# Optimization experiments

Measured on AMD Instinct MI355X. Metric: run time of the kernel, lower is better.

Reference implementation:

```python
import jax, jax.numpy as jnp
import numpy as np


def _2div(arr):
    arr_res = arr.copy()
    arr_pieces = []
    pa = 0
    st = 0
    needdivcnt = 0
    for i, a in enumerate(arr):
        if a != pa:
            arr_pieces.append([st, i])
            if i - st != 1:
                needdivcnt += 1
            pa = a
            st = i
    arr_pieces.append([st, len(arr)])
    if len(arr) - st != 1:
        needdivcnt += 1
    offset = range(len(arr_pieces), len(arr_pieces) + needdivcnt)
    p = 0
    for arr_p in arr_pieces:
        length = arr_p[1] - arr_p[0]
        if length == 1:
            continue
        half_len = int(np.ceil(length / 2))
        for j in range(arr_p[0] + half_len, arr_p[1]):
            arr_res[j] = offset[p]
        p += 1
    return arr_res


def get_division_tree(n_agents):
    agent2divitreeindex = np.arange(n_agents)
    np.random.shuffle(agent2divitreeindex)
    max_div = np.ceil(np.log2(n_agents)).astype(int)
    levels = np.zeros(shape=(max_div + 1, n_agents), dtype=int)
    for ith in range(1, len(levels)):
        levels[ith, :] = _2div(levels[ith - 1, :])
    res_levels = levels.copy()
    for i, idx in enumerate(agent2divitreeindex):
        res_levels[:, i] = levels[:, idx]
    return res_levels


def setup_inputs() -> dict:
    B, A, H, NACT = 2048, 50, 512, 64
    F = H + A  # in-features of first Linear (hidden + one-hot agent id)
    np.random.seed(0)
    div_tree = get_division_tree(A)
    routing = jnp.asarray(div_tree[-1], dtype=jnp.int32)  # max_level routing: agent -> net index
    key = jax.random.key(0)
    k0, k1, k2 = jax.random.split(key, 3)
    x_in = jax.random.normal(k0, (B, A, H), dtype=jnp.float32)
    # stacked per-net parameters (n_nets == n_agent independent 2-layer MLPs)
    W1 = jax.random.normal(k1, (A, F, H), dtype=jnp.float32) * (1.0 / np.sqrt(F))
    b1 = jnp.zeros((A, H), dtype=jnp.float32)
    W2 = jax.random.normal(k2, (A, H, NACT), dtype=jnp.float32) * (1.0 / np.sqrt(H))
    b2 = jnp.zeros((A, NACT), dtype=jnp.float32)
    return {"x_in": x_in, "W1": W1, "b1": b1, "W2": W2, "b2": b2, "routing": routing}


def reference(x_in, W1, b1, W2, b2, routing):
    # x_in: [B, A, H]; routing: [A] int (which net each agent uses)
    B, A, H = x_in.shape
    # add_onehot_id_at_last_dim: append agent-id one-hot -> [B, A, H+A]
    onehot = jnp.broadcast_to(jnp.eye(A, dtype=x_in.dtype), (B, A, A))
    x0 = jnp.concatenate([x_in, onehot], axis=-1)
    # gather routed expert weights per agent
    W1r, b1r = W1[routing], b1[routing]   # [A, H+A, H], [A, H]
    W2r, b2r = W2[routing], b2[routing]   # [A, H, NACT], [A, NACT]
    h = jax.nn.relu(jnp.einsum('baf,afh->bah', x0, W1r) + b1r)
    out = jnp.einsum('bah,ahn->ban', h, W2r) + b2r  # [B, A, NACT]
    return out
```

## Files before the change

### kernel.cpp

```cpp
#include <hip/hip_runtime.h>

typedef __attribute__((ext_vector_type(8))) short bf16x8;
typedef __attribute__((ext_vector_type(4))) float f32x4;
typedef __attribute__((ext_vector_type(4))) unsigned short u16x4;
typedef __attribute__((ext_vector_type(8))) unsigned short u16x8;

#define B_ 2048
#define A_ 50
#define H_ 512
#define NACT_ 64
#define F_ 562
#define BM_ 128
#define BK_ 32
#define NSTEP_ (H_ / BK_)
#define W1LD_ (BK_ + 8)
#define HLD_ (H_ + 8)

#define WS_W1T 0
#define WS_W2T ((size_t)A_ * H_ * H_ * 2)
#define WS_B1 (WS_W2T + (size_t)A_ * NACT_ * H_ * 2)
#define WS_B2 (WS_B1 + (size_t)A_ * H_ * 4)

static __device__ __forceinline__ unsigned short f2bf(float f) {
  unsigned int u = __builtin_bit_cast(unsigned int, f);
  u += 0x7fffu + ((u >> 16) & 1u);
  return (unsigned short)(u >> 16);
}

static __device__ __forceinline__ void gld_lds16(const unsigned short* src,
                                                 unsigned short* dst) {
  __builtin_amdgcn_global_load_lds(
      (const __attribute__((address_space(1))) unsigned int*)(const void*)src,
      (__attribute__((address_space(3))) unsigned int*)(void*)dst, 16, 0, 0);
}

static __device__ __forceinline__ int clamp_r(int r) {
  return r < 0 ? 0 : (r > A_ - 1 ? A_ - 1 : r);
}

__global__ void prep_w1(const float* __restrict__ w1,
                        const int* __restrict__ routing,
                        unsigned short* __restrict__ w1t) {
  const int bid = blockIdx.x;
  const int a = bid / 64;
  const int tile = bid - a * 64;
  const int tk = tile & 7, tj = tile >> 3;
  const int k0 = tk * 64, j0 = tj * 64;
  const int r = clamp_r(routing[a]);
  __shared__ float tl[64][65];
  const int t = threadIdx.x;
  const int c = t & 63, q = t >> 6;
#pragma unroll
  for (int i = 0; i < 16; ++i) {
    const int kl = q + i * 4;
    tl[kl][c] = w1[((size_t)r * F_ + k0 + kl) * H_ + j0 + c];
  }
  __syncthreads();
#pragma unroll
  for (int i = 0; i < 16; ++i) {
    const int jl = q + i * 4;
    w1t[((size_t)a * H_ + j0 + jl) * H_ + k0 + c] = f2bf(tl[c][jl]);
  }
}

__global__ void prep_w2(const float* __restrict__ w2,
                        const int* __restrict__ routing,
                        unsigned short* __restrict__ w2t) {
  const int bid = blockIdx.x;
  const int a = bid >> 3;
  const int tk = bid & 7;
  const int k0 = tk * 64;
  const int r = clamp_r(routing[a]);
  __shared__ float tl[64][65];
  const int t = threadIdx.x;
  const int c = t & 63, q = t >> 6;
#pragma unroll
  for (int i = 0; i < 16; ++i) {
    const int kl = q + i * 4;
    tl[kl][c] = w2[((size_t)r * H_ + k0 + kl) * NACT_ + c];
  }
  __syncthreads();
#pragma unroll
  for (int i = 0; i < 16; ++i) {
    const int nl = q + i * 4;
    w2t[((size_t)a * NACT_ + nl) * H_ + k0 + c] = f2bf(tl[c][nl]);
  }
}

__global__ void prep_bias(const float* __restrict__ w1,
                          const float* __restrict__ b1,
                          const float* __restrict__ b2,
                          const int* __restrict__ routing,
                          float* __restrict__ bias1, float* __restrict__ bias2) {
  const int a = blockIdx.x;
  const int t = threadIdx.x;
  const int r = clamp_r(routing[a]);
  bias1[a * H_ + t] = b1[(size_t)r * H_ + t] + w1[((size_t)r * F_ + H_ + a) * H_ + t];
  if (t < NACT_) bias2[a * NACT_ + t] = b2[r * NACT_ + t];
}

__global__ __launch_bounds__(512, 2) void divtree_main(
    const float* __restrict__ x, const unsigned short* __restrict__ w1t,
    const unsigned short* __restrict__ w2t, const float* __restrict__ bias1,
    const float* __restrict__ bias2, float* __restrict__ out) {
  __shared__ union {
    struct {
      unsigned short w1[2][H_ * W1LD_];
      unsigned short xs[2][BM_ * W1LD_];
    } st;
    unsigned short h[BM_ * HLD_];
  } sm;

  const int bid = blockIdx.x;
  const int swz = (bid & 7) * 100 + (bid >> 3);
  const int a = swz >> 4;
  const int mblk = swz & 15;
  const int b0 = mblk * BM_;

  const int tid = threadIdx.x;
  const int lane = tid & 63;
  const int w = tid >> 6;
  const int l16 = lane & 15;
  const int lk = lane >> 4;

  const int wj = (w & 3) * 128;
  const int wm = (w >> 2) * 64;

  const unsigned short* w1ta = w1t + (size_t)a * H_ * H_;

  const int xrow = tid >> 2;
  const int xc = (tid & 3) * 8;
  const float* xbase =
      x + ((size_t)b0 * A_ + (size_t)a) * H_ + (size_t)xrow * (A_ * H_) + xc;

  f32x4 acc[8][4];
#pragma unroll
  for (int i = 0; i < 8; ++i)
#pragma unroll
    for (int j = 0; j < 4; ++j) acc[i][j] = (f32x4){0.f, 0.f, 0.f, 0.f};

  f32x4 xv0, xv1;

  {
    xv0 = *(const f32x4*)(xbase);
    xv1 = *(const f32x4*)(xbase + 4);
#pragma unroll
    for (int i = 0; i < 5; ++i) {
      const int chunk = i * 512 + tid;
      const int j = chunk / 5;
      const int part = chunk - j * 5;
      const unsigned short* src =
          (part < 4) ? (w1ta + (size_t)j * H_ + part * 8) : w1ta;
      unsigned short* dst = sm.st.w1[0] + (size_t)(i * 512 + (w << 6)) * 8;
      gld_lds16(src, dst);
    }
    u16x8 v;
#pragma unroll
    for (int e = 0; e < 4; ++e) v[e] = f2bf(xv0[e]);
#pragma unroll
    for (int e = 0; e < 4; ++e) v[4 + e] = f2bf(xv1[e]);
    *(u16x8*)(sm.st.xs[0] + xrow * W1LD_ + xc) = v;
  }
  __syncthreads();

  int cur = 0;
  for (int t = 0; t < NSTEP_; ++t) {
    const bool pf = (t + 1 < NSTEP_);
    if (pf) {
      const float* p = xbase + (t + 1) * BK_;
      xv0 = *(const f32x4*)p;
      xv1 = *(const f32x4*)(p + 4);
      const int k0 = (t + 1) * BK_;
#pragma unroll
      for (int i = 0; i < 5; ++i) {
        const int chunk = i * 512 + tid;
        const int j = chunk / 5;
        const int part = chunk - j * 5;
        const unsigned short* src =
            (part < 4) ? (w1ta + (size_t)j * H_ + k0 + part * 8) : w1ta;
        unsigned short* dst =
            sm.st.w1[cur ^ 1] + (size_t)(i * 512 + (w << 6)) * 8;
        gld_lds16(src, dst);
      }
    }
    const unsigned short* w1s = sm.st.w1[cur];
    const unsigned short* xss = sm.st.xs[cur];
    bf16x8 afr[8], bfr[4];
#pragma unroll
    for (int jf = 0; jf < 8; ++jf)
      afr[jf] = *(const bf16x8*)(w1s + (wj + jf * 16 + l16) * W1LD_ + lk * 8);
#pragma unroll
    for (int mf = 0; mf < 4; ++mf)
      bfr[mf] = *(const bf16x8*)(xss + (wm + mf * 16 + l16) * W1LD_ + lk * 8);
#pragma unroll
    for (int jf = 0; jf < 8; ++jf)
#pragma unroll
      for (int mf = 0; mf < 4; ++mf)
        acc[jf][mf] = __builtin_amdgcn_mfma_f32_16x16x32_bf16(
            afr[jf], bfr[mf], acc[jf][mf], 0, 0, 0);
    if (pf) {
      u16x8 v;
#pragma unroll
      for (int e = 0; e < 4; ++e) v[e] = f2bf(xv0[e]);
#pragma unroll
      for (int e = 0; e < 4; ++e) v[4 + e] = f2bf(xv1[e]);
      *(u16x8*)(sm.st.xs[cur ^ 1] + xrow * W1LD_ + xc) = v;
    }
    __syncthreads();
    cur ^= 1;
  }

  const float* b1p = bias1 + a * H_;
#pragma unroll
  for (int jf = 0; jf < 8; ++jf) {
    const f32x4 bv = *(const f32x4*)(b1p + wj + jf * 16 + lk * 4);
#pragma unroll
    for (int mf = 0; mf < 4; ++mf) {
      u16x4 hv;
#pragma unroll
      for (int r = 0; r < 4; ++r) {
        float f = acc[jf][mf][r] + bv[r];
        f = f > 0.f ? f : 0.f;
        hv[r] = f2bf(f);
      }
      const int m = wm + mf * 16 + l16;
      const int j0 = wj + jf * 16 + lk * 4;
      *(u16x4*)(sm.h + (size_t)m * HLD_ + j0) = hv;
    }
  }
  __syncthreads();

  const int n2 = (w & 3) * 16;
  const int m2 = (w >> 2) * 64;
  const unsigned short* w2p =
      w2t + ((size_t)a * NACT_ + n2 + l16) * H_ + lk * 8;
  f32x4 acc2[4];
#pragma unroll
  for (int mf = 0; mf < 4; ++mf) acc2[mf] = (f32x4){0.f, 0.f, 0.f, 0.f};
#pragma unroll
  for (int ks = 0; ks < 16; ++ks) {
    const bf16x8 bf2 = *(const bf16x8*)(w2p + ks * 32);
#pragma unroll
    for (int mf = 0; mf < 4; ++mf) {
      const bf16x8 af2 = *(const bf16x8*)(
          sm.h + (size_t)(m2 + mf * 16 + l16) * HLD_ + ks * 32 + lk * 8);
      acc2[mf] = __builtin_amdgcn_mfma_f32_16x16x32_bf16(af2, bf2, acc2[mf],
                                                         0, 0, 0);
    }
  }
  const float b2v = bias2[a * NACT_ + n2 + l16];
#pragma unroll
  for (int mf = 0; mf < 4; ++mf)
#pragma unroll
    for (int r = 0; r < 4; ++r) {
      const int m = m2 + mf * 16 + lk * 4 + r;
      out[((size_t)(b0 + m) * A_ + a) * NACT_ + n2 + l16] = acc2[mf][r] + b2v;
    }
}

extern "C" void kernel_launch(void* const* d_in, const int* in_sizes, int n_in,
                              void* d_out, int out_size, void* d_ws,
                              size_t ws_size, hipStream_t stream) {
  const float* x = (const float*)d_in[0];
  const float* w1 = (const float*)d_in[1];
  const float* b1 = (const float*)d_in[2];
  const float* w2 = (const float*)d_in[3];
  const float* b2 = (const float*)d_in[4];
  const int* routing = (const int*)d_in[5];
  float* out = (float*)d_out;

  char* ws = (char*)d_ws;
  unsigned short* w1t = (unsigned short*)(ws + WS_W1T);
  unsigned short* w2t = (unsigned short*)(ws + WS_W2T);
  float* bias1 = (float*)(ws + WS_B1);
  float* bias2 = (float*)(ws + WS_B2);

  prep_w1<<<A_ * 64, 256, 0, stream>>>(w1, routing, w1t);
  prep_w2<<<A_ * 8, 256, 0, stream>>>(w2, routing, w2t);
  prep_bias<<<A_, 512, 0, stream>>>(w1, b1, b2, routing, bias1, bias2);
  divtree_main<<<A_ * (B_ / BM_), 512, 0, stream>>>(x, w1t, w2t, bias1, bias2,
                                                    out);
}
```

Baseline: 157.9 us.

## Halve batch tile, pre-tile W1 with XOR swizzle, drop LDS padding for occupancy

The prep kernel now writes W1 in a K-tiled layout where each 32-wide K slice is contiguous and 8-element chunks are XOR-swizzled by row. The main kernel can then load each stage with plain linear global-to-LDS copies and read fragments without bank conflicts, and no padded LDS rows are needed. The batch tile drops from 128 to 64 rows, which doubles the grid and halves accumulator registers, and launch bounds are raised to allow 4 blocks per CU. In exchange each block reloads the full W1 slice for half as many rows, doubling W1 traffic through L2.

```diff
diff --git a/kernel.cpp b/kernel.cpp
--- a/kernel.cpp
+++ b/kernel.cpp
@@ -3,18 +3,15 @@
 typedef __attribute__((ext_vector_type(8))) short bf16x8;
 typedef __attribute__((ext_vector_type(4))) float f32x4;
 typedef __attribute__((ext_vector_type(4))) unsigned short u16x4;
-typedef __attribute__((ext_vector_type(8))) unsigned short u16x8;
 
 #define B_ 2048
 #define A_ 50
 #define H_ 512
 #define NACT_ 64
 #define F_ 562
-#define BM_ 128
+#define BM_ 64
 #define BK_ 32
 #define NSTEP_ (H_ / BK_)
-#define W1LD_ (BK_ + 8)
-#define HLD_ (H_ + 8)
 
 #define WS_W1T 0
 #define WS_W2T ((size_t)A_ * H_ * H_ * 2)
@@ -59,7 +56,14 @@
 #pragma unroll
   for (int i = 0; i < 16; ++i) {
     const int jl = q + i * 4;
-    w1t[((size_t)a * H_ + j0 + jl) * H_ + k0 + c] = f2bf(tl[c][jl]);
+    const int j = j0 + jl;
+    const int k = k0 + c;
+    const int ts = k >> 5;
+    const int sub = (k >> 3) & 3;
+    const int elem = k & 7;
+    const size_t idx = (((size_t)a * 16 + ts) * H_ + j) * 32 +
+                       (size_t)((sub ^ (j & 3)) * 8 + elem);
+    w1t[idx] = f2bf(tl[c][jl]);
   }
 }
 
@@ -99,22 +103,22 @@
   if (t < NACT_) bias2[a * NACT_ + t] = b2[r * NACT_ + t];
 }
 
-__global__ __launch_bounds__(512, 2) void divtree_main(
+__global__ __launch_bounds__(512, 4) void divtree_main(
     const float* __restrict__ x, const unsigned short* __restrict__ w1t,
     const unsigned short* __restrict__ w2t, const float* __restrict__ bias1,
     const float* __restrict__ bias2, float* __restrict__ out) {
   __shared__ union {
     struct {
-      unsigned short w1[2][H_ * W1LD_];
-      unsigned short xs[2][BM_ * W1LD_];
+      unsigned short w1[2][H_ * BK_];
+      unsigned short xs[2][BM_ * BK_];
     } st;
-    unsigned short h[BM_ * HLD_];
+    unsigned short h[BM_ * H_];
   } sm;
 
   const int bid = blockIdx.x;
-  const int swz = (bid & 7) * 100 + (bid >> 3);
-  const int a = swz >> 4;
-  const int mblk = swz & 15;
+  const int swz = (bid & 7) * 200 + (bid >> 3);
+  const int a = swz >> 5;
+  const int mblk = swz & 31;
   const int b0 = mblk * BM_;
 
   const int tid = threadIdx.x;
@@ -122,44 +126,41 @@
   const int w = tid >> 6;
   const int l16 = lane & 15;
   const int lk = lane >> 4;
-
-  const int wj = (w & 3) * 128;
-  const int wm = (w >> 2) * 64;
-
-  const unsigned short* w1ta = w1t + (size_t)a * H_ * H_;
-
-  const int xrow = tid >> 2;
-  const int xc = (tid & 3) * 8;
+  const int sxor = lk ^ (l16 & 3);
+
+  const int wj = w * 64;
+
+  const unsigned short* w1ta = w1t + (size_t)a * (H_ * H_);
+
+  const int xrow = tid >> 3;
+  const int xq = tid & 7;
   const float* xbase =
-      x + ((size_t)b0 * A_ + (size_t)a) * H_ + (size_t)xrow * (A_ * H_) + xc;
-
-  f32x4 acc[8][4];
-#pragma unroll
-  for (int i = 0; i < 8; ++i)
+      x + ((size_t)(b0 + xrow) * A_ + (size_t)a) * H_ + (size_t)xq * 4;
+  const int xs_off = xrow * BK_ + ((xq >> 1) ^ (xrow & 3)) * 8 + (xq & 1) * 4;
+
+  const int afr_base = (wj + l16) * BK_ + sxor * 8;
+  const int bfr_base = l16 * BK_ + sxor * 8;
+
+  f32x4 acc[4][4];
+#pragma unroll
+  for (int i = 0; i < 4; ++i)
 #pragma unroll
     for (int j = 0; j < 4; ++j) acc[i][j] = (f32x4){0.f, 0.f, 0.f, 0.f};
 
-  f32x4 xv0, xv1;
+  f32x4 xv;
 
   {
-    xv0 = *(const f32x4*)(xbase);
-    xv1 = *(const f32x4*)(xbase + 4);
-#pragma unroll
-    for (int i = 0; i < 5; ++i) {
-      const int chunk = i * 512 + tid;
-      const int j = chunk / 5;
-      const int part = chunk - j * 5;
-      const unsigned short* src =
-          (part < 4) ? (w1ta + (size_t)j * H_ + part * 8) : w1ta;
+    xv = *(const f32x4*)(xbase);
+#pragma unroll
+    for (int i = 0; i < 4; ++i) {
+      const unsigned short* src = w1ta + ((size_t)(i * 512 + tid) << 3);
       unsigned short* dst = sm.st.w1[0] + (size_t)(i * 512 + (w << 6)) * 8;
       gld_lds16(src, dst);
     }
-    u16x8 v;
-#pragma unroll
-    for (int e = 0; e < 4; ++e) v[e] = f2bf(xv0[e]);
-#pragma unroll
-    for (int e = 0; e < 4; ++e) v[4 + e] = f2bf(xv1[e]);
-    *(u16x8*)(sm.st.xs[0] + xrow * W1LD_ + xc) = v;
+    u16x4 v;
+#pragma unroll
+    for (int e = 0; e < 4; ++e) v[e] = f2bf(xv[e]);
+    *(u16x4*)(sm.st.xs[0] + xs_off) = v;
   }
   __syncthreads();
 
@@ -167,17 +168,11 @@
   for (int t = 0; t < NSTEP_; ++t) {
     const bool pf = (t + 1 < NSTEP_);
     if (pf) {
-      const float* p = xbase + (t + 1) * BK_;
-      xv0 = *(const f32x4*)p;
-      xv1 = *(const f32x4*)(p + 4);
-      const int k0 = (t + 1) * BK_;
-#pragma unroll
-      for (int i = 0; i < 5; ++i) {
-        const int chunk = i * 512 + tid;
-        const int j = chunk / 5;
-        const int part = chunk - j * 5;
-        const unsigned short* src =
-            (part < 4) ? (w1ta + (size_t)j * H_ + k0 + part * 8) : w1ta;
+      xv = *(const f32x4*)(xbase + (t + 1) * BK_);
+      const unsigned short* wsrc = w1ta + (size_t)(t + 1) * (H_ * BK_);
+#pragma unroll
+      for (int i = 0; i < 4; ++i) {
+        const unsigned short* src = wsrc + ((size_t)(i * 512 + tid) << 3);
         unsigned short* dst =
             sm.st.w1[cur ^ 1] + (size_t)(i * 512 + (w << 6)) * 8;
         gld_lds16(src, dst);
@@ -185,26 +180,24 @@
     }
     const unsigned short* w1s = sm.st.w1[cur];
     const unsigned short* xss = sm.st.xs[cur];
-    bf16x8 afr[8], bfr[4];
-#pragma unroll
-    for (int jf = 0; jf < 8; ++jf)
-      afr[jf] = *(const bf16x8*)(w1s + (wj + jf * 16 + l16) * W1LD_ + lk * 8);
+    bf16x8 afr[4], bfr[4];
+#pragma unroll
+    for (int jf = 0; jf < 4; ++jf)
+      afr[jf] = *(const bf16x8*)(w1s + afr_base + jf * (16 * BK_));
 #pragma unroll
     for (int mf = 0; mf < 4; ++mf)
-      bfr[mf] = *(const bf16x8*)(xss + (wm + mf * 16 + l16) * W1LD_ + lk * 8);
-#pragma unroll
-    for (int jf = 0; jf < 8; ++jf)
+      bfr[mf] = *(const bf16x8*)(xss + bfr_base + mf * (16 * BK_));
+#pragma unroll
+    for (int jf = 0; jf < 4; ++jf)
 #pragma unroll
       for (int mf = 0; mf < 4; ++mf)
         acc[jf][mf] = __builtin_amdgcn_mfma_f32_16x16x32_bf16(
             afr[jf], bfr[mf], acc[jf][mf], 0, 0, 0);
     if (pf) {
-      u16x8 v;
-#pragma unroll
-      for (int e = 0; e < 4; ++e) v[e] = f2bf(xv0[e]);
-#pragma unroll
-      for (int e = 0; e < 4; ++e) v[4 + e] = f2bf(xv1[e]);
-      *(u16x8*)(sm.st.xs[cur ^ 1] + xrow * W1LD_ + xc) = v;
+      u16x4 v;
+#pragma unroll
+      for (int e = 0; e < 4; ++e) v[e] = f2bf(xv[e]);
+      *(u16x4*)(sm.st.xs[cur ^ 1] + xs_off) = v;
     }
     __syncthreads();
     cur ^= 1;
@@ -212,8 +205,10 @@
 
   const float* b1p = bias1 + a * H_;
 #pragma unroll
-  for (int jf = 0; jf < 8; ++jf) {
+  for (int jf = 0; jf < 4; ++jf) {
     const f32x4 bv = *(const f32x4*)(b1p + wj + jf * 16 + lk * 4);
+    const int cbase = (wj >> 3) + jf * 2 + (lk >> 1);
+    const int half4 = (lk & 1) * 4;
 #pragma unroll
     for (int mf = 0; mf < 4; ++mf) {
       u16x4 hv;
@@ -223,38 +218,39 @@
         f = f > 0.f ? f : 0.f;
         hv[r] = f2bf(f);
       }
-      const int m = wm + mf * 16 + l16;
-      const int j0 = wj + jf * 16 + lk * 4;
-      *(u16x4*)(sm.h + (size_t)m * HLD_ + j0) = hv;
-    }
-  }
-  __syncthreads();
-
-  const int n2 = (w & 3) * 16;
-  const int m2 = (w >> 2) * 64;
+      const int m = mf * 16 + l16;
+      const int off = m * H_ + (cbase ^ (l16 & 7)) * 8 + half4;
+      *(u16x4*)(sm.h + off) = hv;
+    }
+  }
+  __syncthreads();
+
+  const int m0 = (w & 1) * 32;
+  const int n0 = (w >> 1) * 16;
   const unsigned short* w2p =
-      w2t + ((size_t)a * NACT_ + n2 + l16) * H_ + lk * 8;
-  f32x4 acc2[4];
-#pragma unroll
-  for (int mf = 0; mf < 4; ++mf) acc2[mf] = (f32x4){0.f, 0.f, 0.f, 0.f};
-#pragma unroll
-  for (int ks = 0; ks < 16; ++ks) {
-    const bf16x8 bf2 = *(const bf16x8*)(w2p + ks * 32);
-#pragma unroll
-    for (int mf = 0; mf < 4; ++mf) {
-      const bf16x8 af2 = *(const bf16x8*)(
-          sm.h + (size_t)(m2 + mf * 16 + l16) * HLD_ + ks * 32 + lk * 8);
+      w2t + ((size_t)a * NACT_ + n0 + l16) * H_ + lk * 8;
+  f32x4 acc2[2];
+  acc2[0] = (f32x4){0.f, 0.f, 0.f, 0.f};
+  acc2[1] = (f32x4){0.f, 0.f, 0.f, 0.f};
+#pragma unroll
+  for (int kf = 0; kf < 16; ++kf) {
+    const bf16x8 bf2 = *(const bf16x8*)(w2p + kf * 32);
+#pragma unroll
+    for (int mf = 0; mf < 2; ++mf) {
+      const int row = m0 + mf * 16 + l16;
+      const int off = row * H_ + (((kf * 4 + lk) ^ (l16 & 7))) * 8;
+      const bf16x8 af2 = *(const bf16x8*)(sm.h + off);
       acc2[mf] = __builtin_amdgcn_mfma_f32_16x16x32_bf16(af2, bf2, acc2[mf],
                                                          0, 0, 0);
     }
   }
-  const float b2v = bias2[a * NACT_ + n2 + l16];
-#pragma unroll
-  for (int mf = 0; mf < 4; ++mf)
+  const float b2v = bias2[a * NACT_ + n0 + l16];
+#pragma unroll
+  for (int mf = 0; mf < 2; ++mf)
 #pragma unroll
     for (int r = 0; r < 4; ++r) {
-      const int m = m2 + mf * 16 + lk * 4 + r;
-      out[((size_t)(b0 + m) * A_ + a) * NACT_ + n2 + l16] = acc2[mf][r] + b2v;
+      const int m = m0 + mf * 16 + lk * 4 + r;
+      out[((size_t)(b0 + m) * A_ + a) * NACT_ + n0 + l16] = acc2[mf][r] + b2v;
     }
 }
 
```

After: 153.2 us. 1.03x faster.
